# Kernel optimization log

Hardware: AMD Instinct MI355X
Metric: run time of the kernel (lower is better)

Reference implementation:

```python
import jax, jax.numpy as jnp
import numpy as np

D_K = 64  # per-head key dim, used for 1/sqrt(d_k) scaling


def setup_inputs() -> dict:
    key = jax.random.key(0)
    ks = jax.random.split(key, 9)
    B, S, D, H, DK, DV = 2, 4096, 512, 8, 64, 64
    s = 0.02
    return {
        "x": jax.random.normal(ks[0], (B, S, D), dtype=jnp.float32),
        "Wq": jax.random.normal(ks[1], (H, D, DK), dtype=jnp.float32) * s,
        "bq": jax.random.normal(ks[2], (H, DK), dtype=jnp.float32) * s,
        "Wk": jax.random.normal(ks[3], (H, D, DK), dtype=jnp.float32) * s,
        "bk": jax.random.normal(ks[4], (H, DK), dtype=jnp.float32) * s,
        "Wv": jax.random.normal(ks[5], (H, D, DV), dtype=jnp.float32) * s,
        "bv": jax.random.normal(ks[6], (H, DV), dtype=jnp.float32) * s,
        "Wo": jax.random.normal(ks[7], (H * DV, D), dtype=jnp.float32) * s,
        "bo": jax.random.normal(ks[8], (D,), dtype=jnp.float32) * s,
    }


def reference(x, Wq, bq, Wk, bk, Wv, bv, Wo, bo):
    # Per-head projections, vectorized over heads: [B,H,S,dk/dv]
    q = jnp.einsum("bsd,hdk->bhsk", x, Wq) + bq[None, :, None, :]
    k = jnp.einsum("bsd,hdk->bhsk", x, Wk) + bk[None, :, None, :]
    v = jnp.einsum("bsd,hdv->bhsv", x, Wv) + bv[None, :, None, :]
    # Scaled dot-product attention (no mask; dropout inactive at eval)
    scores = jnp.einsum("bhsk,bhtk->bhst", q, k) / jnp.sqrt(jnp.float32(D_K))
    attn = jax.nn.softmax(scores, axis=-1)
    o = jnp.einsum("bhst,bhtv->bhsv", attn, v)
    # Concat heads along feature dim: [B,S,H*dv]
    B, H, S, DV = o.shape
    concat = jnp.transpose(o, (0, 2, 1, 3)).reshape(B, S, H * DV)
    return concat @ Wo + bo
```

## Files before the change

kernel.cpp:

```cpp
#include <hip/hip_runtime.h>
#include <hip/hip_bf16.h>

typedef __attribute__((ext_vector_type(8))) short bf16x8;
typedef __attribute__((ext_vector_type(4))) float f32x4;
typedef __attribute__((ext_vector_type(16))) float f32x16;
typedef __attribute__((ext_vector_type(4))) unsigned short u16x4;
typedef __attribute__((ext_vector_type(4))) unsigned int u32x4;

#define NB 2
#define NS 4096
#define ND 512
#define NH 8

__device__ __forceinline__ unsigned short f2bf(float f) {
  unsigned int u = __float_as_uint(f);
  u += 0x7fffu + ((u >> 16) & 1u);
  return (unsigned short)(u >> 16);
}

__device__ __forceinline__ float bf2f(unsigned short h) {
  return __uint_as_float(((unsigned)h) << 16);
}

__device__ __forceinline__ float exp2_hw(float x) {
  float r;
  asm("v_exp_f32 %0, %1" : "=v"(r) : "v"(x));
  return r;
}

__device__ __forceinline__ unsigned cvtpk(float lo, float hi) {
  unsigned r;
  asm("v_cvt_pk_bf16_f32 %0, %1, %2" : "=v"(r) : "v"(lo), "v"(hi));
  return r;
}

__device__ __forceinline__ void swap32(unsigned& a, unsigned& b) {
  asm("v_permlane32_swap_b32 %0, %1" : "+v"(a), "+v"(b));
}

__device__ __forceinline__ bf16x8 mkfrag(unsigned w0, unsigned w1,
                                         unsigned w2, unsigned w3) {
  u32x4 u = {w0, w1, w2, w3};
  return __builtin_bit_cast(bf16x8, u);
}

__device__ __forceinline__ void gload_lds16(const unsigned short* g,
                                            unsigned short* l) {
  __builtin_amdgcn_global_load_lds(
      (const __attribute__((address_space(1))) unsigned int*)g,
      (__attribute__((address_space(3))) unsigned int*)l, 16, 0, 0);
}

__global__ void pack_kernel(const float* __restrict__ x,
                            const float* __restrict__ Wq,
                            const float* __restrict__ Wk,
                            const float* __restrict__ Wv,
                            const float* __restrict__ Wo,
                            unsigned short* __restrict__ x_bf,
                            unsigned short* __restrict__ w3,
                            unsigned short* __restrict__ wo_t)
{
  int idx = blockIdx.x * 256 + threadIdx.x;
  const int NX4 = NB * NS * ND / 4;
  const int NW = 512 * 512;
  if (idx < NX4) {
    const float4 f = ((const float4*)x)[idx];
    u16x4 o;
    o[0] = f2bf(f.x); o[1] = f2bf(f.y); o[2] = f2bf(f.z); o[3] = f2bf(f.w);
    ((u16x4*)x_bf)[idx] = o;
  } else if (idx < NX4 + 3 * NW) {
    int j = idx - NX4;
    int p = j / NW;
    int r = j - p * NW;
    int n = r >> 9, d = r & 511;
    int h = n >> 6, o = n & 63;
    const float* W = (p == 0) ? Wq : (p == 1) ? Wk : Wv;
    w3[j] = f2bf(W[(h * 512 + d) * 64 + o]);
  } else if (idx < NX4 + 4 * NW) {
    int j = idx - NX4 - 3 * NW;
    int n = j >> 9, kk = j & 511;
    wo_t[j] = f2bf(Wo[kk * 512 + n]);
  }
}

template <int MODE>
__global__ void gemm_bt(const unsigned short* __restrict__ A,
                        const unsigned short* __restrict__ Bm,
                        const float* __restrict__ b0,
                        const float* __restrict__ b1,
                        const float* __restrict__ b2,
                        unsigned short* __restrict__ qo,
                        unsigned short* __restrict__ ko,
                        unsigned short* __restrict__ vo,
                        float* __restrict__ fo) {
  __shared__ unsigned short Al[128 * 32];
  __shared__ unsigned short Bl[128 * 32];
  const int t = threadIdx.x;
  const int m0 = blockIdx.x * 128;
  const int n0 = blockIdx.y * 128;
  const int lane = t & 63;
  const int w = t >> 6;
  const int wm = w >> 1, wn = w & 1;
  const int c = lane & 15, g = lane >> 4;

  f32x4 acc[4][4];
#pragma unroll
  for (int i = 0; i < 4; ++i)
#pragma unroll
    for (int j = 0; j < 4; ++j) acc[i][j] = (f32x4){0.f, 0.f, 0.f, 0.f};

  const int srow = t >> 1, sseg = (t & 1) * 16;
  const unsigned short* Ap = A + (size_t)(m0 + srow) * 512 + sseg;
  const unsigned short* Bp = Bm + (size_t)(n0 + srow) * 512 + sseg;
  unsigned short* Alp = &Al[srow * 32 + sseg];
  unsigned short* Blp = &Bl[srow * 32 + sseg];

  for (int k0 = 0; k0 < 512; k0 += 32) {
    bf16x8 ra0 = *(const bf16x8*)(Ap + k0);
    bf16x8 ra1 = *(const bf16x8*)(Ap + k0 + 8);
    bf16x8 rb0 = *(const bf16x8*)(Bp + k0);
    bf16x8 rb1 = *(const bf16x8*)(Bp + k0 + 8);
    __syncthreads();
    *(bf16x8*)(Alp) = ra0;
    *(bf16x8*)(Alp + 8) = ra1;
    *(bf16x8*)(Blp) = rb0;
    *(bf16x8*)(Blp + 8) = rb1;
    __syncthreads();
    bf16x8 af[4], bfr[4];
#pragma unroll
    for (int mf = 0; mf < 4; ++mf)
      af[mf] = *(const bf16x8*)&Al[(wm * 64 + mf * 16 + c) * 32 + g * 8];
#pragma unroll
    for (int nf = 0; nf < 4; ++nf)
      bfr[nf] = *(const bf16x8*)&Bl[(wn * 64 + nf * 16 + c) * 32 + g * 8];
#pragma unroll
    for (int mf = 0; mf < 4; ++mf)
#pragma unroll
      for (int nf = 0; nf < 4; ++nf)
        acc[mf][nf] = __builtin_amdgcn_mfma_f32_16x16x32_bf16(
            af[mf], bfr[nf], acc[mf][nf], 0, 0, 0);
  }

  if (MODE == 0) {
    const int proj = n0 >> 9;
    const float* bias = proj == 0 ? b0 : (proj == 1 ? b1 : b2);
    unsigned short* dst01 = proj == 0 ? qo : ko;
    const float scale = proj == 0 ? 0.18033688011112042f : 1.0f;
#pragma unroll
    for (int nf = 0; nf < 4; ++nf) {
      const int col5 = (n0 + wn * 64 + nf * 16 + c) & 511;
      const int h = col5 >> 6, o = col5 & 63;
      const float bb = bias[col5];
#pragma unroll
      for (int mf = 0; mf < 4; ++mf) {
#pragma unroll
        for (int r = 0; r < 4; ++r) {
          const int m = m0 + wm * 64 + mf * 16 + g * 4 + r;
          const int b = m >> 12, s = m & 4095;
          const unsigned short hb = f2bf((acc[mf][nf][r] + bb) * scale);
          if (proj < 2)
            dst01[((size_t)((b * NH + h) * NS + s)) * 64 + o] = hb;
          else
            vo[((size_t)((b * NH + h) * 64 + o)) * NS + s] = hb;
        }
      }
    }
  } else {
#pragma unroll
    for (int nf = 0; nf < 4; ++nf) {
      const int col = n0 + wn * 64 + nf * 16 + c;
      const float bb = b0[col];
#pragma unroll
      for (int mf = 0; mf < 4; ++mf) {
#pragma unroll
        for (int r = 0; r < 4; ++r) {
          const int m = m0 + wm * 64 + mf * 16 + g * 4 + r;
          fo[(size_t)m * 512 + col] = acc[mf][nf][r] + bb;
        }
      }
    }
  }
}

__device__ __forceinline__ void softmax_qset_fm(f32x16& pA, f32x16& pB,
                                                float& l_, bf16x8* pb) {
#pragma unroll
  for (int r = 0; r < 16; ++r) {
    pA[r] = exp2_hw(pA[r]);
    pB[r] = exp2_hw(pB[r]);
  }
  float s[8];
#pragma unroll
  for (int r = 0; r < 8; ++r)
    s[r] = (pA[r] + pA[r + 8]) + (pB[r] + pB[r + 8]);
  float rs = ((s[0] + s[1]) + (s[2] + s[3])) + ((s[4] + s[5]) + (s[6] + s[7]));
  rs += __shfl_xor(rs, 32, 64);
  l_ += rs;
  unsigned g0[8], g1[8];
#pragma unroll
  for (int gg = 0; gg < 8; ++gg) {
    g0[gg] = cvtpk(pA[2 * gg], pA[2 * gg + 1]);
    g1[gg] = cvtpk(pB[2 * gg], pB[2 * gg + 1]);
  }
  unsigned a1, b1, c1, d1;
  a1 = g0[0]; b1 = g0[2]; swap32(a1, b1);
  c1 = g0[1]; d1 = g0[3]; swap32(c1, d1);
  pb[0] = mkfrag(a1, c1, b1, d1);
  a1 = g0[4]; b1 = g0[6]; swap32(a1, b1);
  c1 = g0[5]; d1 = g0[7]; swap32(c1, d1);
  pb[1] = mkfrag(a1, c1, b1, d1);
  a1 = g1[0]; b1 = g1[2]; swap32(a1, b1);
  c1 = g1[1]; d1 = g1[3]; swap32(c1, d1);
  pb[2] = mkfrag(a1, c1, b1, d1);
  a1 = g1[4]; b1 = g1[6]; swap32(a1, b1);
  c1 = g1[5]; d1 = g1[7]; swap32(c1, d1);
  pb[3] = mkfrag(a1, c1, b1, d1);
}

template <int SPLITS>
__global__ __launch_bounds__(256, 1) void attn_kernel(
    const unsigned short* __restrict__ q,
    const unsigned short* __restrict__ k,
    const unsigned short* __restrict__ vt,
    unsigned short* __restrict__ cc,
    unsigned short* __restrict__ op,
    float* __restrict__ ml)
{
  union SMemU {
    struct { unsigned short Kl[2][4096]; unsigned short Vl[2][4096]; } kv;
    unsigned short Ol[4][32][68];
  };
  __shared__ SMemU sm;
  const int t = threadIdx.x;
  const int w = t >> 6, lane = t & 63;
  const int col = lane & 31, hi = lane >> 5;
  const int bh = blockIdx.y & 15;
  const int sp = blockIdx.y >> 4;
  const int b = bh >> 3, h = bh & 7;
  const int q0 = blockIdx.x * 256 + w * 64;
  const int kbase = sp * (NS / SPLITS);

  const unsigned short* qh = q + (size_t)bh * NS * 64;
  const unsigned short* kh = k + (size_t)bh * NS * 64;
  const unsigned short* vh = vt + (size_t)bh * 64 * NS;

  bf16x8 qf[2][4];
#pragma unroll
  for (int qs = 0; qs < 2; ++qs)
#pragma unroll
    for (int c = 0; c < 4; ++c)
      qf[qs][c] = *(const bf16x8*)&qh[(size_t)(q0 + qs * 32 + col) * 64 +
                                      c * 16 + hi * 8];

  const int rl = lane >> 3, chn = lane & 7;
  const int lk = rl * 64 + ((chn ^ (rl & 7)) << 3);
  const int lv = rl * NS + ((chn ^ (rl & 7)) << 3);

  f32x16 ot[4];
#pragma unroll
  for (int i = 0; i < 4; ++i)
#pragma unroll
    for (int r = 0; r < 16; ++r) ot[i][r] = 0.f;
  float l_[2] = {0.f, 0.f};

  const int NT = NS / (64 * SPLITS);

  {
    const unsigned short* gk = kh + (size_t)(kbase + w * 16) * 64;
    const unsigned short* gv = vh + (size_t)(w * 16) * NS + kbase;
    gload_lds16(gk + lk, &sm.kv.Kl[0][w * 1024]);
    gload_lds16(gk + lk + 512, &sm.kv.Kl[0][w * 1024 + 512]);
    gload_lds16(gv + lv, &sm.kv.Vl[0][w * 1024]);
    gload_lds16(gv + lv + 8 * NS, &sm.kv.Vl[0][w * 1024 + 512]);
    __syncthreads();
  }

  for (int it = 0; it < NT; ++it) {
    const int cur = it & 1;
    if (it + 1 < NT) {
      const unsigned short* gk =
          kh + (size_t)(kbase + (it + 1) * 64 + w * 16) * 64;
      const unsigned short* gv =
          vh + (size_t)(w * 16) * NS + kbase + (it + 1) * 64;
      gload_lds16(gk + lk, &sm.kv.Kl[cur ^ 1][w * 1024]);
      gload_lds16(gk + lk + 512, &sm.kv.Kl[cur ^ 1][w * 1024 + 512]);
      gload_lds16(gv + lv, &sm.kv.Vl[cur ^ 1][w * 1024]);
      gload_lds16(gv + lv + 8 * NS, &sm.kv.Vl[cur ^ 1][w * 1024 + 512]);
    }

    bf16x8 kfr[2][4];
#pragma unroll
    for (int c = 0; c < 4; ++c) {
      const int cidx = (((2 * c + hi) ^ (col & 7)) << 3);
      kfr[0][c] = *(const bf16x8*)&sm.kv.Kl[cur][col * 64 + cidx];
      kfr[1][c] = *(const bf16x8*)&sm.kv.Kl[cur][(col + 32) * 64 + cidx];
    }

    f32x16 p0, p1;
#pragma unroll
    for (int r = 0; r < 16; ++r) { p0[r] = 0.f; p1[r] = 0.f; }
    __builtin_amdgcn_s_setprio(1);
#pragma unroll
    for (int c = 0; c < 4; ++c) {
      p0 = __builtin_amdgcn_mfma_f32_32x32x16_bf16(kfr[0][c], qf[0][c], p0, 0, 0, 0);
      p1 = __builtin_amdgcn_mfma_f32_32x32x16_bf16(kfr[1][c], qf[0][c], p1, 0, 0, 0);
    }
    __builtin_amdgcn_s_setprio(0);

    bf16x8 pb0[4];
    softmax_qset_fm(p0, p1, l_[0], pb0);

    f32x16 p2, p3;
#pragma unroll
    for (int r = 0; r < 16; ++r) { p2[r] = 0.f; p3[r] = 0.f; }
    __builtin_amdgcn_s_setprio(1);
#pragma unroll
    for (int c = 0; c < 4; ++c) {
      p2 = __builtin_amdgcn_mfma_f32_32x32x16_bf16(kfr[0][c], qf[1][c], p2, 0, 0, 0);
      p3 = __builtin_amdgcn_mfma_f32_32x32x16_bf16(kfr[1][c], qf[1][c], p3, 0, 0, 0);
    }
    __builtin_amdgcn_s_setprio(0);

    bf16x8 vfr[2][4];
#pragma unroll
    for (int ks = 0; ks < 4; ++ks) {
      const int cidx = (((2 * ks + hi) ^ (col & 7)) << 3);
      vfr[0][ks] = *(const bf16x8*)&sm.kv.Vl[cur][col * 64 + cidx];
      vfr[1][ks] = *(const bf16x8*)&sm.kv.Vl[cur][(col + 32) * 64 + cidx];
    }
    __builtin_amdgcn_s_setprio(1);
#pragma unroll
    for (int ks = 0; ks < 4; ++ks) {
      ot[0] = __builtin_amdgcn_mfma_f32_32x32x16_bf16(vfr[0][ks], pb0[ks], ot[0], 0, 0, 0);
      ot[1] = __builtin_amdgcn_mfma_f32_32x32x16_bf16(vfr[1][ks], pb0[ks], ot[1], 0, 0, 0);
    }
    __builtin_amdgcn_s_setprio(0);

    bf16x8 pb1[4];
    softmax_qset_fm(p2, p3, l_[1], pb1);
    __builtin_amdgcn_s_setprio(1);
#pragma unroll
    for (int ks = 0; ks < 4; ++ks) {
      ot[2] = __builtin_amdgcn_mfma_f32_32x32x16_bf16(vfr[0][ks], pb1[ks], ot[2], 0, 0, 0);
      ot[3] = __builtin_amdgcn_mfma_f32_32x32x16_bf16(vfr[1][ks], pb1[ks], ot[3], 0, 0, 0);
    }
    __builtin_amdgcn_s_setprio(0);

    __syncthreads();
  }

#pragma unroll
  for (int qs = 0; qs < 2; ++qs) {
    const float inv = (SPLITS == 1) ? (1.0f / l_[qs]) : 1.0f;
#pragma unroll
    for (int r = 0; r < 16; ++r) {
      const int dvb = (r & 3) + 8 * (r >> 2) + 4 * hi;
      sm.Ol[w][col][dvb] = f2bf(ot[qs * 2][r] * inv);
      sm.Ol[w][col][dvb + 32] = f2bf(ot[qs * 2 + 1][r] * inv);
    }
    if (SPLITS > 1 && hi == 0)
      ml[(size_t)(sp * 16 + bh) * NS + q0 + qs * 32 + col] = l_[qs];
    asm volatile("s_waitcnt lgkmcnt(0)" ::: "memory");
    const int row = lane >> 1;
#pragma unroll
    for (int p = 0; p < 4; ++p) {
      const int chunk = (lane & 1) + 2 * p;
      bf16x8 vv = *(const bf16x8*)&sm.Ol[w][row][chunk * 8];
      if (SPLITS == 1)
        *(bf16x8*)&cc[((size_t)(b * NS + q0 + qs * 32 + row)) * 512 + h * 64 +
                      chunk * 8] = vv;
      else
        *(bf16x8*)&op[((size_t)(sp * 16 + bh) * NS + q0 + qs * 32 + row) * 64 +
                      chunk * 8] = vv;
    }
    asm volatile("s_waitcnt lgkmcnt(0)" ::: "memory");
  }
}

template <int SPLITS>
__global__ void combine_kernel(const unsigned short* __restrict__ op,
                               const float* __restrict__ ml,
                               unsigned short* __restrict__ cc) {
  const int id = blockIdx.x * 256 + threadIdx.x;
  const int chunk = id & 7;
  const int qq = (id >> 3) & 4095;
  const int bh = id >> 15;
  const int b = bh >> 3, h = bh & 7;
  float lsum = 0.f;
#pragma unroll
  for (int sp = 0; sp < SPLITS; ++sp)
    lsum += ml[(size_t)(sp * 16 + bh) * NS + qq];
  const float invl = 1.0f / lsum;
  float acc[8];
#pragma unroll
  for (int j = 0; j < 8; ++j) acc[j] = 0.f;
#pragma unroll
  for (int sp = 0; sp < SPLITS; ++sp) {
    const bf16x8 o =
        *(const bf16x8*)&op[((size_t)(sp * 16 + bh) * NS + qq) * 64 + chunk * 8];
#pragma unroll
    for (int j = 0; j < 8; ++j) acc[j] += bf2f((unsigned short)o[j]);
  }
  bf16x8 out;
#pragma unroll
  for (int j = 0; j < 8; ++j) out[j] = (short)f2bf(acc[j] * invl);
  *(bf16x8*)&cc[((size_t)(b * NS + qq)) * 512 + h * 64 + chunk * 8] = out;
}

extern "C" void kernel_launch(void* const* d_in, const int* in_sizes, int n_in,
                              void* d_out, int out_size, void* d_ws, size_t ws_size,
                              hipStream_t stream) {
  const float* x  = (const float*)d_in[0];
  const float* Wq = (const float*)d_in[1];
  const float* bq = (const float*)d_in[2];
  const float* Wk = (const float*)d_in[3];
  const float* bk = (const float*)d_in[4];
  const float* Wv = (const float*)d_in[5];
  const float* bv = (const float*)d_in[6];
  const float* Wo = (const float*)d_in[7];
  const float* bo = (const float*)d_in[8];

  unsigned char* ws = (unsigned char*)d_ws;
  unsigned short* x_bf = (unsigned short*)(ws);
  unsigned short* w3   = (unsigned short*)(ws + 8388608);
  unsigned short* wo_t = (unsigned short*)(ws + 9961472);
  unsigned short* qb   = (unsigned short*)(ws + 10485760);
  unsigned short* kb   = (unsigned short*)(ws + 18874368);
  unsigned short* vb   = (unsigned short*)(ws + 27262976);
  unsigned short* op   = (unsigned short*)(ws + 35651584);
  unsigned short* cc   = x_bf;

  const size_t need4 = 35651584ull + 4ull * 8388608 + 4ull * 16 * 4096 * 4;
  const size_t need2 = 35651584ull + 2ull * 8388608 + 2ull * 16 * 4096 * 4;

  pack_kernel<<<8192, 256, 0, stream>>>(x, Wq, Wk, Wv, Wo, x_bf, w3, wo_t);
  gemm_bt<0><<<dim3(64, 12), 256, 0, stream>>>(x_bf, w3, bq, bk, bv, qb, kb, vb,
                                               nullptr);
  if (ws_size >= need4) {
    float* mlp = (float*)(ws + 35651584 + 4ull * 8388608);
    attn_kernel<4><<<dim3(16, 64), 256, 0, stream>>>(qb, kb, vb, nullptr, op,
                                                     mlp);
    combine_kernel<4><<<2048, 256, 0, stream>>>(op, mlp, cc);
  } else if (ws_size >= need2) {
    float* mlp = (float*)(ws + 35651584 + 2ull * 8388608);
    attn_kernel<2><<<dim3(16, 32), 256, 0, stream>>>(qb, kb, vb, nullptr, op,
                                                     mlp);
    combine_kernel<2><<<2048, 256, 0, stream>>>(op, mlp, cc);
  } else {
    attn_kernel<1><<<dim3(16, 16), 256, 0, stream>>>(qb, kb, vb, cc, nullptr,
                                                     nullptr);
  }
  gemm_bt<1><<<dim3(64, 4), 256, 0, stream>>>(cc, wo_t, bo, nullptr, nullptr,
                                              nullptr, nullptr, nullptr,
                                              (float*)d_out);
}
```

Before: 167.6 us.

## Triple-buffer K/V tiles with vmcnt waits and drop the 4-way key split

The attention kernel moves from double to triple buffering of K/V tiles in LDS. Tiles are prefetched two iterations ahead, and the per-iteration __syncthreads is replaced by an s_waitcnt vmcnt plus a single s_barrier at the top of the loop. The host also drops the SPLITS=4 path and uses the 2-way key split. This cuts the grid in half, lengthens each block's loop and lowers combine traffic. Costs: LDS use rises to 48KB per block, fewer blocks may leave CUs idle, and the hardcoded vmcnt(4) assumes exactly four outstanding loads per issue.

```diff
diff --git a/kernel.cpp b/kernel.cpp
--- a/kernel.cpp
+++ b/kernel.cpp
@@ -227,7 +227,7 @@
     float* __restrict__ ml)
 {
   union SMemU {
-    struct { unsigned short Kl[2][4096]; unsigned short Vl[2][4096]; } kv;
+    struct { unsigned short Kl[3][4096]; unsigned short Vl[3][4096]; } kv;
     unsigned short Ol[4][32][68];
   };
   __shared__ SMemU sm;
@@ -256,6 +256,15 @@
   const int lk = rl * 64 + ((chn ^ (rl & 7)) << 3);
   const int lv = rl * NS + ((chn ^ (rl & 7)) << 3);
 
+  auto ISSUE = [&](int tile, int bi) {
+    const unsigned short* gk = kh + (size_t)(kbase + tile * 64 + w * 16) * 64;
+    const unsigned short* gv = vh + (size_t)(w * 16) * NS + kbase + tile * 64;
+    gload_lds16(gk + lk, &sm.kv.Kl[bi][w * 1024]);
+    gload_lds16(gk + lk + 512, &sm.kv.Kl[bi][w * 1024 + 512]);
+    gload_lds16(gv + lv, &sm.kv.Vl[bi][w * 1024]);
+    gload_lds16(gv + lv + 8 * NS, &sm.kv.Vl[bi][w * 1024 + 512]);
+  };
+
   f32x16 ot[4];
 #pragma unroll
   for (int i = 0; i < 4; ++i)
@@ -265,27 +274,21 @@
 
   const int NT = NS / (64 * SPLITS);
 
-  {
-    const unsigned short* gk = kh + (size_t)(kbase + w * 16) * 64;
-    const unsigned short* gv = vh + (size_t)(w * 16) * NS + kbase;
-    gload_lds16(gk + lk, &sm.kv.Kl[0][w * 1024]);
-    gload_lds16(gk + lk + 512, &sm.kv.Kl[0][w * 1024 + 512]);
-    gload_lds16(gv + lv, &sm.kv.Vl[0][w * 1024]);
-    gload_lds16(gv + lv + 8 * NS, &sm.kv.Vl[0][w * 1024 + 512]);
-    __syncthreads();
-  }
-
+  ISSUE(0, 0);
+  if (NT > 1) ISSUE(1, 1);
+
+  int cur = 0;
   for (int it = 0; it < NT; ++it) {
-    const int cur = it & 1;
-    if (it + 1 < NT) {
-      const unsigned short* gk =
-          kh + (size_t)(kbase + (it + 1) * 64 + w * 16) * 64;
-      const unsigned short* gv =
-          vh + (size_t)(w * 16) * NS + kbase + (it + 1) * 64;
-      gload_lds16(gk + lk, &sm.kv.Kl[cur ^ 1][w * 1024]);
-      gload_lds16(gk + lk + 512, &sm.kv.Kl[cur ^ 1][w * 1024 + 512]);
-      gload_lds16(gv + lv, &sm.kv.Vl[cur ^ 1][w * 1024]);
-      gload_lds16(gv + lv + 8 * NS, &sm.kv.Vl[cur ^ 1][w * 1024 + 512]);
+    if (it + 1 < NT)
+      asm volatile("s_waitcnt vmcnt(4)" ::: "memory");
+    else
+      asm volatile("s_waitcnt vmcnt(0)" ::: "memory");
+    __builtin_amdgcn_s_barrier();
+    __builtin_amdgcn_sched_barrier(0);
+    if (it + 2 < NT) {
+      int b2 = cur + 2;
+      if (b2 >= 3) b2 -= 3;
+      ISSUE(it + 2, b2);
     }
 
     bf16x8 kfr[2][4];
@@ -346,8 +349,10 @@
     }
     __builtin_amdgcn_s_setprio(0);
 
-    __syncthreads();
-  }
+    cur = (cur + 1 == 3) ? 0 : cur + 1;
+  }
+
+  __syncthreads();
 
 #pragma unroll
   for (int qs = 0; qs < 2; ++qs) {
@@ -430,18 +435,12 @@
   unsigned short* op   = (unsigned short*)(ws + 35651584);
   unsigned short* cc   = x_bf;
 
-  const size_t need4 = 35651584ull + 4ull * 8388608 + 4ull * 16 * 4096 * 4;
   const size_t need2 = 35651584ull + 2ull * 8388608 + 2ull * 16 * 4096 * 4;
 
   pack_kernel<<<8192, 256, 0, stream>>>(x, Wq, Wk, Wv, Wo, x_bf, w3, wo_t);
   gemm_bt<0><<<dim3(64, 12), 256, 0, stream>>>(x_bf, w3, bq, bk, bv, qb, kb, vb,
                                                nullptr);
-  if (ws_size >= need4) {
-    float* mlp = (float*)(ws + 35651584 + 4ull * 8388608);
-    attn_kernel<4><<<dim3(16, 64), 256, 0, stream>>>(qb, kb, vb, nullptr, op,
-                                                     mlp);
-    combine_kernel<4><<<2048, 256, 0, stream>>>(op, mlp, cc);
-  } else if (ws_size >= need2) {
+  if (ws_size >= need2) {
     float* mlp = (float*)(ws + 35651584 + 2ull * 8388608);
     attn_kernel<2><<<dim3(16, 32), 256, 0, stream>>>(qb, kb, vb, nullptr, op,
                                                      mlp);
```

New measurement: 163.2 us. 2.6% less time.
